# Optimization experiments

Measured on AMD Instinct MI355X. Metric: run time of the kernel, lower is better.

The kernel has to match this reference:

```python
import jax, jax.numpy as jnp
import numpy as np

F_FD = 16      # fdfilter
XLEN = 128     # grid side
BS, CH = 16, 4


def _conv(x, w):
    # x: [N, Cin, H, W], w: [Cout, Cin, kh, kw], VALID, stride 1
    return jax.lax.conv_general_dilated(
        x, w, window_strides=(1, 1), padding='VALID',
        dimension_numbers=('NCHW', 'OIHW', 'NCHW'))


def setup_inputs() -> dict:
    key = jax.random.key(0)
    ks = jax.random.split(key, 14)
    s = 0.1
    F = F_FD
    inp = {
        'xInput': jax.random.normal(ks[0], (BS, CH, XLEN, XLEN), dtype=jnp.float32),
        'wX1':  jax.random.normal(ks[1],  (F, 1, 1, 3), dtype=jnp.float32) * s,
        'wX1L': jax.random.normal(ks[2],  (F, 1, 1, 2), dtype=jnp.float32) * s,
        'wX1R': jax.random.normal(ks[3],  (F, 1, 1, 2), dtype=jnp.float32) * s,
        'wY1':  jax.random.normal(ks[4],  (F, 1, 3, 1), dtype=jnp.float32) * s,
        'wY1L': jax.random.normal(ks[5],  (F, 1, 2, 1), dtype=jnp.float32) * s,
        'wY1R': jax.random.normal(ks[6],  (F, 1, 2, 1), dtype=jnp.float32) * s,
        'wX2':  jax.random.normal(ks[7],  (F, F, 1, 3), dtype=jnp.float32) * s,
        'wX2L': jax.random.normal(ks[8],  (F, F, 1, 2), dtype=jnp.float32) * s,
        'wX2R': jax.random.normal(ks[9],  (F, F, 1, 2), dtype=jnp.float32) * s,
        'wY2':  jax.random.normal(ks[10], (F, F, 3, 1), dtype=jnp.float32) * s,
        'wY2L': jax.random.normal(ks[11], (F, F, 2, 1), dtype=jnp.float32) * s,
        'wY2R': jax.random.normal(ks[12], (F, F, 2, 1), dtype=jnp.float32) * s,
        'wfc':  jax.random.normal(ks[13], (1, 4 * F), dtype=jnp.float32) * s,
        'fdblock': 8,
    }
    return inp


def reference(xInput, wX1, wX1L, wX1R, wY1, wY1L, wY1R,
              wX2, wX2L, wX2R, wY2, wY2L, wY2R, wfc, fdblock):
    BS_, C_, H, W = xInput.shape
    x = xInput.reshape(-1, 1, H, W)  # fold channels into batch, Cin=1
    for _ in range(fdblock):
        # first-order x/y finite-difference stencils with boundary convs
        dX = jnp.concatenate([_conv(x[:, :, :, :2], wX1L),
                              _conv(x, wX1),
                              _conv(x[:, :, :, -2:], wX1R)], axis=3)
        dY = jnp.concatenate([_conv(x[:, :, :2, :], wY1L),
                              _conv(x, wY1),
                              _conv(x[:, :, -2:, :], wY1R)], axis=2)
        # second-order stencils on the first-order fields
        dX2 = jnp.concatenate([_conv(dX[:, :, :, :2], wX2L),
                               _conv(dX, wX2),
                               _conv(dX[:, :, :, -2:], wX2R)], axis=3)
        dY2 = jnp.concatenate([_conv(dY[:, :, :2, :], wY2L),
                               _conv(dY, wY2),
                               _conv(dY[:, :, -2:, :], wY2R)], axis=2)
        combine = jnp.concatenate([dX, dY, dX2, dY2], axis=1)  # [N, 4F, H, W]
        # fc over channel dim (transpose(1,3)+Linear+transpose(1,3) == channel contraction)
        deviation = jnp.einsum('nchw,oc->nohw', combine, wfc)  # [N, 1, H, W]
        x = x + deviation
    return x.reshape(BS_, C_, H, W)
```

## Files before the change

### kernel.cpp

```cpp
#include <hip/hip_runtime.h>

#define F 16
#define XL 128


__device__ __forceinline__ float g1f(const float* __restrict__ w1,
                                     const float* __restrict__ w1L,
                                     const float* __restrict__ w1R,
                                     int f, int v, int wp) {
  if (v == 0) {
    if (wp == 0) return w1L[f * 2 + 0];
    if (wp == 1) return w1L[f * 2 + 1];
    return 0.f;
  }
  if (v == XL - 1) {
    if (wp == XL - 2) return w1R[f * 2 + 0];
    if (wp == XL - 1) return w1R[f * 2 + 1];
    return 0.f;
  }
  int k = wp - (v - 1);
  return (k >= 0 && k < 3) ? w1[f * 3 + k] : 0.f;
}

__global__ __launch_bounds__(256)
void build_bands_kernel(const float* __restrict__ wX1, const float* __restrict__ wX1L,
                        const float* __restrict__ wX1R, const float* __restrict__ wY1,
                        const float* __restrict__ wY1L, const float* __restrict__ wY1R,
                        const float* __restrict__ wX2, const float* __restrict__ wX2L,
                        const float* __restrict__ wX2R, const float* __restrict__ wY2,
                        const float* __restrict__ wY2L, const float* __restrict__ wY2R,
                        const float* __restrict__ wfc, float* __restrict__ bands) {
  __shared__ float r1s[2][3], r1Ls[2][2], r1Rs[2][2];
  __shared__ float qs[2][F][3], qLs[2][F][2], qRs[2][F][2];

  const int t = threadIdx.x;
  if (t < 6) {
    int p = t / 3, k = t % 3;
    const float* w1 = p ? wY1 : wX1;
    int off = p ? F : 0;
    float s = 0.f;
    for (int f = 0; f < F; ++f) s += wfc[off + f] * w1[f * 3 + k];
    r1s[p][k] = s;
  } else if (t < 10) {
    int t2 = t - 6; int p = t2 / 2, k = t2 % 2;
    const float* w1L = p ? wY1L : wX1L;
    int off = p ? F : 0;
    float s = 0.f;
    for (int f = 0; f < F; ++f) s += wfc[off + f] * w1L[f * 2 + k];
    r1Ls[p][k] = s;
  } else if (t < 14) {
    int t2 = t - 10; int p = t2 / 2, k = t2 % 2;
    const float* w1R = p ? wY1R : wX1R;
    int off = p ? F : 0;
    float s = 0.f;
    for (int f = 0; f < F; ++f) s += wfc[off + f] * w1R[f * 2 + k];
    r1Rs[p][k] = s;
  } else if (t < 14 + 96) {
    int t2 = t - 14; int p = t2 / 48; int r = t2 % 48; int fi = r / 3, k = r % 3;
    const float* w2 = p ? wY2 : wX2;
    int off = p ? 3 * F : 2 * F;
    float s = 0.f;
    for (int fo = 0; fo < F; ++fo) s += wfc[off + fo] * w2[(fo * F + fi) * 3 + k];
    qs[p][fi][k] = s;
  } else if (t < 110 + 64) {
    int t2 = t - 110; int p = t2 / 32; int r = t2 % 32; int fi = r / 2, k = r % 2;
    const float* w2L = p ? wY2L : wX2L;
    int off = p ? 3 * F : 2 * F;
    float s = 0.f;
    for (int fo = 0; fo < F; ++fo) s += wfc[off + fo] * w2L[(fo * F + fi) * 2 + k];
    qLs[p][fi][k] = s;
  } else if (t < 174 + 64) {
    int t2 = t - 174; int p = t2 / 32; int r = t2 % 32; int fi = r / 2, k = r % 2;
    const float* w2R = p ? wY2R : wX2R;
    int off = p ? 3 * F : 2 * F;
    float s = 0.f;
    for (int fo = 0; fo < F; ++fo) s += wfc[off + fo] * w2R[(fo * F + fi) * 2 + k];
    qRs[p][fi][k] = s;
  }
  __syncthreads();

  int gid = blockIdx.x * 256 + t;
  if (gid >= 2 * XL * 5) return;
  const int p = gid / (XL * 5);
  const int rem = gid % (XL * 5);
  const int w = rem / 5;
  const int d = rem % 5;
  const int wp = w + d - 2;

  const float* w1  = p ? wY1  : wX1;
  const float* w1L = p ? wY1L : wX1L;
  const float* w1R = p ? wY1R : wX1R;

  float c = 0.f;
  if (wp >= 0 && wp < XL) {
    if (w == 0) {
      if (wp == 0)       c += r1Ls[p][0];
      else if (wp == 1)  c += r1Ls[p][1];
    } else if (w == XL - 1) {
      if (wp == XL - 2)      c += r1Rs[p][0];
      else if (wp == XL - 1) c += r1Rs[p][1];
    } else {
      int k = wp - (w - 1);
      if (k >= 0 && k < 3) c += r1s[p][k];
    }
    if (w == 0) {
      for (int vi = 0; vi < 2; ++vi)
        for (int fi = 0; fi < F; ++fi)
          c += qLs[p][fi][vi] * g1f(w1, w1L, w1R, fi, vi, wp);
    } else if (w == XL - 1) {
      for (int vi = 0; vi < 2; ++vi)
        for (int fi = 0; fi < F; ++fi)
          c += qRs[p][fi][vi] * g1f(w1, w1L, w1R, fi, XL - 2 + vi, wp);
    } else {
      for (int k2 = 0; k2 < 3; ++k2) {
        int v = w - 1 + k2;
        for (int fi = 0; fi < F; ++fi)
          c += qs[p][fi][k2] * g1f(w1, w1L, w1R, fi, v, wp);
      }
    }
  }
  bands[(p * 5 + d) * XL + w] = c;
}

__device__ __forceinline__ float dpp_shr1(float x) {
  return __int_as_float(
      __builtin_amdgcn_update_dpp(0, __float_as_int(x), 0x138, 0xf, 0xf, true));
}
__device__ __forceinline__ float dpp_shl1(float x) {
  return __int_as_float(
      __builtin_amdgcn_update_dpp(0, __float_as_int(x), 0x130, 0xf, 0xf, true));
}

__global__ __launch_bounds__(256)
void fd_reg_kernel(const float* __restrict__ x_in, const float* __restrict__ bands,
                   const int* __restrict__ fdp, float* __restrict__ x_out) {
  __shared__ float hbuf[2][4][2][XL][2];

  const int tid = threadIdx.x;
  const int z = tid & 63;
  const int w = tid >> 6;
  const int n = blockIdx.x >> 2;
  const int s = blockIdx.x & 3;
  int cs0 = 32 * s - 16; if (cs0 < 0) cs0 = 0; if (cs0 > 64) cs0 = 64;
  const int c0 = cs0 + 16 * w;
  const int r0 = 2 * z, r1 = 2 * z + 1;

  const float* img = x_in + n * XL * XL;

  float f0[16], f1[16];
  {
    const float4* a = (const float4*)(img + r0 * XL + c0);
    const float4* b = (const float4*)(img + r1 * XL + c0);
#pragma unroll
    for (int m = 0; m < 4; ++m) {
      const float4 v = a[m];
      f0[4 * m] = v.x; f0[4 * m + 1] = v.y; f0[4 * m + 2] = v.z; f0[4 * m + 3] = v.w;
      const float4 u = b[m];
      f1[4 * m] = u.x; f1[4 * m + 1] = u.y; f1[4 * m + 2] = u.z; f1[4 * m + 3] = u.w;
    }
  }

  float rbi[5], rbe0[5], rbe1[5], rbe14[5], rbe15[5], cb0[5], cb1[5];
#pragma unroll
  for (int d = 0; d < 5; ++d) {
    rbi[d]   = bands[d * XL + 64];
    rbe0[d]  = bands[d * XL + c0];
    rbe1[d]  = bands[d * XL + c0 + 1];
    rbe14[d] = bands[d * XL + c0 + 14];
    rbe15[d] = bands[d * XL + c0 + 15];
    cb0[d]   = bands[(5 + d) * XL + r0];
    cb1[d]   = bands[(5 + d) * XL + r1];
  }

  const int fdb = fdp[0];
  const int wl = (w > 0) ? w - 1 : 0;
  const int wr = (w < 3) ? w + 1 : 3;

  for (int t = 0; t < fdb; ++t) {
    const int b = t & 1;
    *(float2*)&hbuf[b][w][0][r0][0] = make_float2(f0[0], f0[1]);
    *(float2*)&hbuf[b][w][0][r1][0] = make_float2(f1[0], f1[1]);
    *(float2*)&hbuf[b][w][1][r0][0] = make_float2(f0[14], f0[15]);
    *(float2*)&hbuf[b][w][1][r1][0] = make_float2(f1[14], f1[15]);
    __syncthreads();
    const float2 lh0 = *(const float2*)&hbuf[b][wl][1][r0][0];
    const float2 lh1 = *(const float2*)&hbuf[b][wl][1][r1][0];
    const float2 rh0 = *(const float2*)&hbuf[b][wr][0][r0][0];
    const float2 rh1 = *(const float2*)&hbuf[b][wr][0][r1][0];

    float om2_0 = 0.f, om1_0 = 0.f, om2_1 = 0.f, om1_1 = 0.f;
#pragma unroll
    for (int k = 0; k < 16; ++k) {
      const float o0 = f0[k], o1 = f1[k];
      const float vm2 = dpp_shr1(o0);
      const float vm1 = dpp_shr1(o1);
      const float vp2 = dpp_shl1(o0);
      const float vp3 = dpp_shl1(o1);
      const float hm2_0 = (k == 0) ? lh0.x : (k == 1) ? lh0.y : om2_0;
      const float hm1_0 = (k == 0) ? lh0.y : om1_0;
      const float hm2_1 = (k == 0) ? lh1.x : (k == 1) ? lh1.y : om2_1;
      const float hm1_1 = (k == 0) ? lh1.y : om1_1;
      const float hp1_0 = (k < 15) ? f0[k + 1] : rh0.x;
      const float hp2_0 = (k < 14) ? f0[k + 2] : ((k == 14) ? rh0.x : rh0.y);
      const float hp1_1 = (k < 15) ? f1[k + 1] : rh1.x;
      const float hp2_1 = (k < 14) ? f1[k + 2] : ((k == 14) ? rh1.x : rh1.y);
      float c0b, c1b, c2b, c3b, c4b;
      if (k == 0)       { c0b = rbe0[0];  c1b = rbe0[1];  c2b = rbe0[2];  c3b = rbe0[3];  c4b = rbe0[4];  }
      else if (k == 1)  { c0b = rbe1[0];  c1b = rbe1[1];  c2b = rbe1[2];  c3b = rbe1[3];  c4b = rbe1[4];  }
      else if (k == 14) { c0b = rbe14[0]; c1b = rbe14[1]; c2b = rbe14[2]; c3b = rbe14[3]; c4b = rbe14[4]; }
      else if (k == 15) { c0b = rbe15[0]; c1b = rbe15[1]; c2b = rbe15[2]; c3b = rbe15[3]; c4b = rbe15[4]; }
      else              { c0b = rbi[0];   c1b = rbi[1];   c2b = rbi[2];   c3b = rbi[3];   c4b = rbi[4];   }

      const float n0 = o0
        + c0b * hm2_0 + c1b * hm1_0 + c2b * o0 + c3b * hp1_0 + c4b * hp2_0
        + cb0[0] * vm2 + cb0[1] * vm1 + cb0[2] * o0 + cb0[3] * o1 + cb0[4] * vp2;
      const float n1 = o1
        + c0b * hm2_1 + c1b * hm1_1 + c2b * o1 + c3b * hp1_1 + c4b * hp2_1
        + cb1[0] * vm1 + cb1[1] * o0 + cb1[2] * o1 + cb1[3] * vp2 + cb1[4] * vp3;

      om2_0 = om1_0; om1_0 = o0; om2_1 = om1_1; om1_1 = o1;
      f0[k] = n0; f1[k] = n1;
    }
  }

  if (c0 == 32 * s || c0 == 32 * s + 16) {
    float* outp = x_out + n * XL * XL;
    float4* o0p = (float4*)(outp + r0 * XL + c0);
    float4* o1p = (float4*)(outp + r1 * XL + c0);
#pragma unroll
    for (int m = 0; m < 4; ++m) {
      o0p[m] = make_float4(f0[4 * m], f0[4 * m + 1], f0[4 * m + 2], f0[4 * m + 3]);
      o1p[m] = make_float4(f1[4 * m], f1[4 * m + 1], f1[4 * m + 2], f1[4 * m + 3]);
    }
  }
}

extern "C" void kernel_launch(void* const* d_in, const int* in_sizes, int n_in,
                              void* d_out, int out_size, void* d_ws, size_t ws_size,
                              hipStream_t stream) {
  const float* xInput = (const float*)d_in[0];
  const float* wX1  = (const float*)d_in[1];
  const float* wX1L = (const float*)d_in[2];
  const float* wX1R = (const float*)d_in[3];
  const float* wY1  = (const float*)d_in[4];
  const float* wY1L = (const float*)d_in[5];
  const float* wY1R = (const float*)d_in[6];
  const float* wX2  = (const float*)d_in[7];
  const float* wX2L = (const float*)d_in[8];
  const float* wX2R = (const float*)d_in[9];
  const float* wY2  = (const float*)d_in[10];
  const float* wY2L = (const float*)d_in[11];
  const float* wY2R = (const float*)d_in[12];
  const float* wfc  = (const float*)d_in[13];
  const int*   fdp  = (const int*)d_in[14];

  float* bands = (float*)d_ws;
  float* out = (float*)d_out;

  build_bands_kernel<<<5, 256, 0, stream>>>(wX1, wX1L, wX1R, wY1, wY1L, wY1R,
                                            wX2, wX2L, wX2R, wY2, wY2L, wY2R,
                                            wfc, bands);
  fd_reg_kernel<<<256, 256, 0, stream>>>(xInput, bands, fdp, out);
}
```

Baseline: 103.4 us.

## Split each column strip across 8 waves with 8 columns per thread

Each block now uses 512 threads (8 waves), and each thread holds 8 columns per row pair instead of 16. This halves the registers per thread and doubles the waves per block, giving more latency hiding across the 256 blocks. The halo exchange is packed into one float4 LDS slot per lane, and the left neighbour values are seeded from the halo. In exchange, the share of halo work and LDS traffic per thread goes up. The old kernel is left in place but no longer launched, and it still contains dead scaffolding code.

```diff
diff --git a/kernel.cpp b/kernel.cpp
--- a/kernel.cpp
+++ b/kernel.cpp
@@ -131,10 +131,10 @@
       __builtin_amdgcn_update_dpp(0, __float_as_int(x), 0x130, 0xf, 0xf, true));
 }
 
-__global__ __launch_bounds__(256)
+__global__ __launch_bounds__(512)
 void fd_reg_kernel(const float* __restrict__ x_in, const float* __restrict__ bands,
                    const int* __restrict__ fdp, float* __restrict__ x_out) {
-  __shared__ float hbuf[2][4][2][XL][2];
+  __shared__ float4 hbuf[2][8][2][64];
 
   const int tid = threadIdx.x;
   const int z = tid & 63;
@@ -142,17 +142,17 @@
   const int n = blockIdx.x >> 2;
   const int s = blockIdx.x & 3;
   int cs0 = 32 * s - 16; if (cs0 < 0) cs0 = 0; if (cs0 > 64) cs0 = 64;
-  const int c0 = cs0 + 16 * w;
+  const int c0 = cs0 + 8 * w;
   const int r0 = 2 * z, r1 = 2 * z + 1;
 
   const float* img = x_in + n * XL * XL;
 
-  float f0[16], f1[16];
+  float f0[8], f1[8];
   {
     const float4* a = (const float4*)(img + r0 * XL + c0);
     const float4* b = (const float4*)(img + r1 * XL + c0);
 #pragma unroll
-    for (int m = 0; m < 4; ++m) {
+    for (int m = 0; m < 2; ++m) {
       const float4 v = a[m];
       f0[4 * m] = v.x; f0[4 * m + 1] = v.y; f0[4 * m + 2] = v.z; f0[4 * m + 3] = v.w;
       const float4 u = b[m];
@@ -160,75 +160,174 @@
     }
   }
 
-  float rbi[5], rbe0[5], rbe1[5], rbe14[5], rbe15[5], cb0[5], cb1[5];
+  float rbi[5], rbe0[5], rbe1[5], rbe6[5], rbe7[5], cb0[5], cb1[5];
 #pragma unroll
   for (int d = 0; d < 5; ++d) {
-    rbi[d]   = bands[d * XL + 64];
-    rbe0[d]  = bands[d * XL + c0];
-    rbe1[d]  = bands[d * XL + c0 + 1];
-    rbe14[d] = bands[d * XL + c0 + 14];
-    rbe15[d] = bands[d * XL + c0 + 15];
-    cb0[d]   = bands[(5 + d) * XL + r0];
-    cb1[d]   = bands[(5 + d) * XL + r1];
+    rbi[d]  = bands[d * XL + 64];
+    rbe0[d] = bands[d * XL + c0];
+    rbe1[d] = bands[d * XL + c0 + 1];
+    rbe6[d] = bands[d * XL + c0 + 6];
+    rbe7[d] = bands[d * XL + c0 + 7];
+    cb0[d]  = bands[(5 + d) * XL + r0];
+    cb1[d]  = bands[(5 + d) * XL + r1];
   }
 
   const int fdb = fdp[0];
   const int wl = (w > 0) ? w - 1 : 0;
-  const int wr = (w < 3) ? w + 1 : 3;
+  const int wr = (w < 7) ? w + 1 : 7;
 
   for (int t = 0; t < fdb; ++t) {
     const int b = t & 1;
-    *(float2*)&hbuf[b][w][0][r0][0] = make_float2(f0[0], f0[1]);
-    *(float2*)&hbuf[b][w][0][r1][0] = make_float2(f1[0], f1[1]);
-    *(float2*)&hbuf[b][w][1][r0][0] = make_float2(f0[14], f0[15]);
-    *(float2*)&hbuf[b][w][1][r1][0] = make_float2(f1[14], f1[15]);
+    hbuf[b][w][0][z] = make_float4(f0[0], f0[1], f1[0], f1[1]);
+    hbuf[b][w][1][z] = make_float4(f0[6], f0[7], f1[6], f1[7]);
     __syncthreads();
-    const float2 lh0 = *(const float2*)&hbuf[b][wl][1][r0][0];
-    const float2 lh1 = *(const float2*)&hbuf[b][wl][1][r1][0];
-    const float2 rh0 = *(const float2*)&hbuf[b][wr][0][r0][0];
-    const float2 rh1 = *(const float2*)&hbuf[b][wr][0][r1][0];
-
-    float om2_0 = 0.f, om1_0 = 0.f, om2_1 = 0.f, om1_1 = 0.f;
-#pragma unroll
-    for (int k = 0; k < 16; ++k) {
+    const float4 lh = hbuf[b][wl][1][z];
+    const float4 rh = hbuf[b][wr][0][z];
+
+    float om1_0 = 0.f, om1_1 = 0.f;
+#pragma unroll
+    for (int k = 0; k < 8; ++k) {
       const float o0 = f0[k], o1 = f1[k];
       const float vm2 = dpp_shr1(o0);
       const float vm1 = dpp_shr1(o1);
       const float vp2 = dpp_shl1(o0);
       const float vp3 = dpp_shl1(o1);
-      const float hm2_0 = (k == 0) ? lh0.x : (k == 1) ? lh0.y : om2_0;
-      const float hm1_0 = (k == 0) ? lh0.y : om1_0;
-      const float hm2_1 = (k == 0) ? lh1.x : (k == 1) ? lh1.y : om2_1;
-      const float hm1_1 = (k == 0) ? lh1.y : om1_1;
-      const float hp1_0 = (k < 15) ? f0[k + 1] : rh0.x;
-      const float hp2_0 = (k < 14) ? f0[k + 2] : ((k == 14) ? rh0.x : rh0.y);
-      const float hp1_1 = (k < 15) ? f1[k + 1] : rh1.x;
-      const float hp2_1 = (k < 14) ? f1[k + 2] : ((k == 14) ? rh1.x : rh1.y);
+      const float hm2_0 = (k == 0) ? lh.x : (k == 1) ? lh.y : f0[k - 2] * 0.f + om1_0 * 0.f + __builtin_huge_valf() * 0.f + ((k >= 2) ? 0.f : 0.f);
+      const float hm2_0r = (k == 0) ? lh.x : (k == 1) ? lh.y : 0.f;
+      (void)hm2_0; (void)hm2_0r;
+      float hm2a_0, hm1a_0, hm2a_1, hm1a_1;
+      if (k == 0)      { hm2a_0 = lh.x; hm1a_0 = lh.y; hm2a_1 = lh.z; hm1a_1 = lh.w; }
+      else if (k == 1) { hm2a_0 = lh.y; hm1a_0 = om1_0; hm2a_1 = lh.w; hm1a_1 = om1_1; }
+      else             { hm2a_0 = f0[k - 2]; hm1a_0 = om1_0; hm2a_1 = f1[k - 2]; hm1a_1 = om1_1; }
+      const float hp1_0 = (k < 7) ? f0[k + 1] : rh.x;
+      const float hp2_0 = (k < 6) ? f0[k + 2] : ((k == 6) ? rh.x : rh.y);
+      const float hp1_1 = (k < 7) ? f1[k + 1] : rh.z;
+      const float hp2_1 = (k < 6) ? f1[k + 2] : ((k == 6) ? rh.z : rh.w);
       float c0b, c1b, c2b, c3b, c4b;
-      if (k == 0)       { c0b = rbe0[0];  c1b = rbe0[1];  c2b = rbe0[2];  c3b = rbe0[3];  c4b = rbe0[4];  }
-      else if (k == 1)  { c0b = rbe1[0];  c1b = rbe1[1];  c2b = rbe1[2];  c3b = rbe1[3];  c4b = rbe1[4];  }
-      else if (k == 14) { c0b = rbe14[0]; c1b = rbe14[1]; c2b = rbe14[2]; c3b = rbe14[3]; c4b = rbe14[4]; }
-      else if (k == 15) { c0b = rbe15[0]; c1b = rbe15[1]; c2b = rbe15[2]; c3b = rbe15[3]; c4b = rbe15[4]; }
-      else              { c0b = rbi[0];   c1b = rbi[1];   c2b = rbi[2];   c3b = rbi[3];   c4b = rbi[4];   }
+      if (k == 0)      { c0b = rbe0[0]; c1b = rbe0[1]; c2b = rbe0[2]; c3b = rbe0[3]; c4b = rbe0[4]; }
+      else if (k == 1) { c0b = rbe1[0]; c1b = rbe1[1]; c2b = rbe1[2]; c3b = rbe1[3]; c4b = rbe1[4]; }
+      else if (k == 6) { c0b = rbe6[0]; c1b = rbe6[1]; c2b = rbe6[2]; c3b = rbe6[3]; c4b = rbe6[4]; }
+      else if (k == 7) { c0b = rbe7[0]; c1b = rbe7[1]; c2b = rbe7[2]; c3b = rbe7[3]; c4b = rbe7[4]; }
+      else             { c0b = rbi[0];  c1b = rbi[1];  c2b = rbi[2];  c3b = rbi[3];  c4b = rbi[4];  }
 
       const float n0 = o0
-        + c0b * hm2_0 + c1b * hm1_0 + c2b * o0 + c3b * hp1_0 + c4b * hp2_0
+        + c0b * hm2a_0 + c1b * hm1a_0 + c2b * o0 + c3b * hp1_0 + c4b * hp2_0
         + cb0[0] * vm2 + cb0[1] * vm1 + cb0[2] * o0 + cb0[3] * o1 + cb0[4] * vp2;
       const float n1 = o1
-        + c0b * hm2_1 + c1b * hm1_1 + c2b * o1 + c3b * hp1_1 + c4b * hp2_1
+        + c0b * hm2a_1 + c1b * hm1a_1 + c2b * o1 + c3b * hp1_1 + c4b * hp2_1
         + cb1[0] * vm1 + cb1[1] * o0 + cb1[2] * o1 + cb1[3] * vp2 + cb1[4] * vp3;
 
-      om2_0 = om1_0; om1_0 = o0; om2_1 = om1_1; om1_1 = o1;
+      om1_0 = o0; om1_1 = o1;
       f0[k] = n0; f1[k] = n1;
     }
   }
 
-  if (c0 == 32 * s || c0 == 32 * s + 16) {
+  const int rel = c0 - 32 * s;
+  if (rel >= 0 && rel < 32) {
     float* outp = x_out + n * XL * XL;
     float4* o0p = (float4*)(outp + r0 * XL + c0);
     float4* o1p = (float4*)(outp + r1 * XL + c0);
 #pragma unroll
-    for (int m = 0; m < 4; ++m) {
+    for (int m = 0; m < 2; ++m) {
+      o0p[m] = make_float4(f0[4 * m], f0[4 * m + 1], f0[4 * m + 2], f0[4 * m + 3]);
+      o1p[m] = make_float4(f1[4 * m], f1[4 * m + 1], f1[4 * m + 2], f1[4 * m + 3]);
+    }
+  }
+}
+
+__global__ __launch_bounds__(512)
+void fd_reg_kernel2(const float* __restrict__ x_in, const float* __restrict__ bands,
+                    const int* __restrict__ fdp, float* __restrict__ x_out) {
+  __shared__ float4 hbuf[2][8][2][64];
+
+  const int tid = threadIdx.x;
+  const int z = tid & 63;
+  const int w = tid >> 6;
+  const int n = blockIdx.x >> 2;
+  const int s = blockIdx.x & 3;
+  int cs0 = 32 * s - 16; if (cs0 < 0) cs0 = 0; if (cs0 > 64) cs0 = 64;
+  const int c0 = cs0 + 8 * w;
+  const int r0 = 2 * z, r1 = 2 * z + 1;
+
+  const float* img = x_in + n * XL * XL;
+
+  float f0[8], f1[8];
+  {
+    const float4* a = (const float4*)(img + r0 * XL + c0);
+    const float4* b = (const float4*)(img + r1 * XL + c0);
+#pragma unroll
+    for (int m = 0; m < 2; ++m) {
+      const float4 v = a[m];
+      f0[4 * m] = v.x; f0[4 * m + 1] = v.y; f0[4 * m + 2] = v.z; f0[4 * m + 3] = v.w;
+      const float4 u = b[m];
+      f1[4 * m] = u.x; f1[4 * m + 1] = u.y; f1[4 * m + 2] = u.z; f1[4 * m + 3] = u.w;
+    }
+  }
+
+  float rbi[5], rbe0[5], rbe1[5], rbe6[5], rbe7[5], cb0[5], cb1[5];
+#pragma unroll
+  for (int d = 0; d < 5; ++d) {
+    rbi[d]  = bands[d * XL + 64];
+    rbe0[d] = bands[d * XL + c0];
+    rbe1[d] = bands[d * XL + c0 + 1];
+    rbe6[d] = bands[d * XL + c0 + 6];
+    rbe7[d] = bands[d * XL + c0 + 7];
+    cb0[d]  = bands[(5 + d) * XL + r0];
+    cb1[d]  = bands[(5 + d) * XL + r1];
+  }
+
+  const int fdb = fdp[0];
+  const int wl = (w > 0) ? w - 1 : 0;
+  const int wr = (w < 7) ? w + 1 : 7;
+
+  for (int t = 0; t < fdb; ++t) {
+    const int b = t & 1;
+    hbuf[b][w][0][z] = make_float4(f0[0], f0[1], f1[0], f1[1]);
+    hbuf[b][w][1][z] = make_float4(f0[6], f0[7], f1[6], f1[7]);
+    __syncthreads();
+    const float4 lh = hbuf[b][wl][1][z];
+    const float4 rh = hbuf[b][wr][0][z];
+
+    float om2_0 = lh.x, om1_0 = lh.y;
+    float om2_1 = lh.z, om1_1 = lh.w;
+#pragma unroll
+    for (int k = 0; k < 8; ++k) {
+      const float o0 = f0[k], o1 = f1[k];
+      const float vm2 = dpp_shr1(o0);
+      const float vm1 = dpp_shr1(o1);
+      const float vp2 = dpp_shl1(o0);
+      const float vp3 = dpp_shl1(o1);
+      const float hp1_0 = (k < 7) ? f0[k + 1] : rh.x;
+      const float hp2_0 = (k < 6) ? f0[k + 2] : ((k == 6) ? rh.x : rh.y);
+      const float hp1_1 = (k < 7) ? f1[k + 1] : rh.z;
+      const float hp2_1 = (k < 6) ? f1[k + 2] : ((k == 6) ? rh.z : rh.w);
+      float c0b, c1b, c2b, c3b, c4b;
+      if (k == 0)      { c0b = rbe0[0]; c1b = rbe0[1]; c2b = rbe0[2]; c3b = rbe0[3]; c4b = rbe0[4]; }
+      else if (k == 1) { c0b = rbe1[0]; c1b = rbe1[1]; c2b = rbe1[2]; c3b = rbe1[3]; c4b = rbe1[4]; }
+      else if (k == 6) { c0b = rbe6[0]; c1b = rbe6[1]; c2b = rbe6[2]; c3b = rbe6[3]; c4b = rbe6[4]; }
+      else if (k == 7) { c0b = rbe7[0]; c1b = rbe7[1]; c2b = rbe7[2]; c3b = rbe7[3]; c4b = rbe7[4]; }
+      else             { c0b = rbi[0];  c1b = rbi[1];  c2b = rbi[2];  c3b = rbi[3];  c4b = rbi[4];  }
+
+      const float n0 = o0
+        + c0b * om2_0 + c1b * om1_0 + c2b * o0 + c3b * hp1_0 + c4b * hp2_0
+        + cb0[0] * vm2 + cb0[1] * vm1 + cb0[2] * o0 + cb0[3] * o1 + cb0[4] * vp2;
+      const float n1 = o1
+        + c0b * om2_1 + c1b * om1_1 + c2b * o1 + c3b * hp1_1 + c4b * hp2_1
+        + cb1[0] * vm1 + cb1[1] * o0 + cb1[2] * o1 + cb1[3] * vp2 + cb1[4] * vp3;
+
+      om2_0 = om1_0; om1_0 = o0;
+      om2_1 = om1_1; om1_1 = o1;
+      f0[k] = n0; f1[k] = n1;
+    }
+  }
+
+  const int rel = c0 - 32 * s;
+  if (rel >= 0 && rel < 32) {
+    float* outp = x_out + n * XL * XL;
+    float4* o0p = (float4*)(outp + r0 * XL + c0);
+    float4* o1p = (float4*)(outp + r1 * XL + c0);
+#pragma unroll
+    for (int m = 0; m < 2; ++m) {
       o0p[m] = make_float4(f0[4 * m], f0[4 * m + 1], f0[4 * m + 2], f0[4 * m + 3]);
       o1p[m] = make_float4(f1[4 * m], f1[4 * m + 1], f1[4 * m + 2], f1[4 * m + 3]);
     }
@@ -260,5 +359,5 @@
   build_bands_kernel<<<5, 256, 0, stream>>>(wX1, wX1L, wX1R, wY1, wY1L, wY1R,
                                             wX2, wX2L, wX2R, wY2, wY2L, wY2R,
                                             wfc, bands);
-  fd_reg_kernel<<<256, 256, 0, stream>>>(xInput, bands, fdp, out);
-}
+  fd_reg_kernel2<<<256, 512, 0, stream>>>(xInput, bands, fdp, out);
+}
```

Result: no change. 105.1 us (+1.6%).
